# Optimization experiments

Measured on AMD Instinct MI355X. Metric: run time of the kernel, lower is better.

## Reference

```python
import jax, jax.numpy as jnp
import numpy as np

N_CLASSES = 18
NMS_PRE = 1000   # test_cfg.nms_pre, per level
K_NMS = 500      # per-class candidates entering greedy NMS
SCORE_THR = 0.01
IOU_THR = 0.5
LEVEL_NS = [600000, 300000, 150000, 75000]


def _decode(points, pred):
    # fcaf3d axis-aligned decode: pred = (dx-, dx+, dy-, dy+, dz-, dz+) >= 0
    cx = points[:, 0] + (pred[:, 1] - pred[:, 0]) / 2
    cy = points[:, 1] + (pred[:, 3] - pred[:, 2]) / 2
    cz = points[:, 2] + (pred[:, 5] - pred[:, 4]) / 2
    w = pred[:, 0] + pred[:, 1]
    l = pred[:, 2] + pred[:, 3]
    h = pred[:, 4] + pred[:, 5]
    return jnp.stack([cx, cy, cz, w, l, h], axis=-1)  # [N, 6]


def _iou3d(b):
    # axis-aligned 3D IoU, b: [K,6] (cx,cy,cz,w,l,h) -> [K,K]
    mn = b[:, :3] - b[:, 3:] / 2
    mx = b[:, :3] + b[:, 3:] / 2
    lt = jnp.maximum(mn[:, None, :], mn[None, :, :])
    rb = jnp.minimum(mx[:, None, :], mx[None, :, :])
    inter = jnp.clip(rb - lt, 0.0).prod(-1)
    vol = jnp.clip(mx - mn, 0.0).prod(-1)
    return inter / (vol[:, None] + vol[None, :] - inter + 1e-6)


def _level(centerness, bbox_pred, cls_score, points):
    # fused score: cls.sigmoid() * centerness.sigmoid()
    scores = jax.nn.sigmoid(cls_score) * jax.nn.sigmoid(centerness)  # [N,C]
    max_scores = scores.max(axis=1)
    _, ids = jax.lax.top_k(max_scores, NMS_PRE)  # per-level prefilter
    bboxes = _decode(points[ids], bbox_pred[ids])  # [NMS_PRE, 6]
    return bboxes, scores[ids]


def _nms_class(boxes, scores):
    # boxes [M,6], scores [M] for one class -> greedy NMS on top K_NMS
    valid = scores > SCORE_THR
    s = jnp.where(valid, scores, -1.0)
    sv, order = jax.lax.top_k(s, K_NMS)  # sorted desc
    b = boxes[order]
    v = sv > SCORE_THR
    iou = _iou3d(b)  # [K,K]
    idx = jnp.arange(K_NMS)

    def body(i, sup):
        alive = jnp.logical_not(sup[i])
        return sup | (alive & (iou[i] > IOU_THR) & (idx > i))

    sup = jax.lax.fori_loop(0, K_NMS, body, jnp.logical_not(v))
    keep = jnp.logical_not(sup) & v
    return b, sv, keep


def _forward(levels):
    mlvl_bboxes, mlvl_scores = [], []
    for (cn, bp, cs, pt) in levels:
        b, s = _level(cn, bp, cs, pt)
        mlvl_bboxes.append(b)
        mlvl_scores.append(s)
    bboxes = jnp.concatenate(mlvl_bboxes)  # [4*NMS_PRE, 6]
    scores = jnp.concatenate(mlvl_scores)  # [4*NMS_PRE, C]
    # per-class NMS (vmap over class dim)
    b, sv, keep = jax.vmap(_nms_class, in_axes=(None, 1))(bboxes, scores)
    labels = jnp.broadcast_to(jnp.arange(N_CLASSES, dtype=jnp.int32)[:, None], sv.shape)
    return (b.reshape(-1, 6), sv.reshape(-1), labels.reshape(-1), keep.reshape(-1))


def setup_inputs() -> dict:
    key = jax.random.key(0)
    out = {}
    for li, n in enumerate(LEVEL_NS):
        k1, k2, k3, k4, key = jax.random.split(key, 5)
        out[f'centerness{li}'] = jax.random.normal(k1, (n, 1), jnp.float32)
        out[f'bbox_pred{li}'] = jax.random.uniform(k2, (n, 6), jnp.float32)  # non-negative distances
        out[f'cls_score{li}'] = jax.random.normal(k3, (n, N_CLASSES), jnp.float32)
        out[f'points{li}'] = jax.random.normal(k4, (n, 3), jnp.float32) * 2.0
    return out


def reference(centerness0, bbox_pred0, cls_score0, points0,
              centerness1, bbox_pred1, cls_score1, points1,
              centerness2, bbox_pred2, cls_score2, points2,
              centerness3, bbox_pred3, cls_score3, points3):
    levels = [
        (centerness0, bbox_pred0, cls_score0, points0),
        (centerness1, bbox_pred1, cls_score1, points1),
        (centerness2, bbox_pred2, cls_score2, points2),
        (centerness3, bbox_pred3, cls_score3, points3),
    ]
    return _forward(levels)
```

## Files before the change

### kernel.cpp

```cpp
#include <hip/hip_runtime.h>
#include <math.h>

#define N_CLASSES 18
#define NMS_PRE   1000
#define K_NMS     500
#define POOL      4000
#define LIST_CAP  2048
#define NREP      16
#define NSUB      16
#define SUBCAP    (LIST_CAP/NSUB)
#define IOU_THR   0.5f
#define SCORE_THR 0.01f

typedef unsigned long long ull;

struct Ptrs {
  const float* cent[4];
  const float* bbox[4];
  const float* cls[4];
  const float* pts[4];
  int off[4];
  int ntot;
};

__device__ __forceinline__ unsigned int fsort(float f){
  unsigned int b = __float_as_uint(f);
  return (b & 0x80000000u) ? ~b : (b | 0x80000000u);
}
__device__ __forceinline__ float fsort_inv(unsigned int k){
  unsigned int b = (k & 0x80000000u) ? (k & 0x7FFFFFFFu) : ~k;
  return __uint_as_float(b);
}
__device__ __forceinline__ float sigmoidf_(float x){
  return 1.0f / (1.0f + expf(-x));
}
__device__ __forceinline__ int level_of(int f, const Ptrs& P){
  return (f >= P.off[3]) ? 3 : (f >= P.off[2]) ? 2 : (f >= P.off[1]) ? 1 : 0;
}

__device__ __forceinline__ ull cx_keep(ull mine, ull part, bool keep_hi){
  ull mx = mine > part ? mine : part;
  ull mn = mine > part ? part : mine;
  return keep_hi ? mx : mn;
}
__device__ __forceinline__ void cxpair(ull &a, ull &b, bool a_hi){
  ull mx = a > b ? a : b;
  ull mn = a > b ? b : a;
  a = a_hi ? mx : mn;
  b = a_hi ? mn : mx;
}

__global__ void __launch_bounds__(256) init_kernel(unsigned int* hist_rep, unsigned int* hist2,
                        unsigned int* scnt, ull* lists, unsigned int* state){
  int tid = blockIdx.x*256 + threadIdx.x;
  int stride = gridDim.x*256;
  for (int j = tid; j < NREP*4*2048; j += stride) hist_rep[j] = 0u;
  for (int j = tid; j < 4*2048; j += stride) hist2[j] = 0u;
  for (int j = tid; j < 4*NSUB*16; j += stride) scnt[j] = 0u;
  for (int j = tid; j < 4*LIST_CAP; j += stride) lists[j] = 0ull;
  if (tid < 4){
    state[2*tid]   = 0u;
    state[2*tid+1] = NMS_PRE;
  }
}

__global__ void __launch_bounds__(512) compute_keys(Ptrs P, unsigned int* keys,
                        unsigned int* hist_rep){
  __shared__ unsigned int lh[2048];
  int t = threadIdx.x;
  for (int j = t; j < 2048; j += 512) lh[j] = 0u;
  int ip = blockIdx.x*512 + t;
  int f  = ip << 1;
  int rep = blockIdx.x & (NREP - 1);
  bool valid = f < P.ntot;
  int f0 = blockIdx.x << 10;
  int fL = min(f0 + 1023, P.ntot - 1);
  bool uni = (level_of(f0, P) == level_of(fL, P)) && (f0 + 1023 < P.ntot);
  int Lb = level_of(f0, P);

  float mA = 0.f, mB = 0.f, cA = 0.f, cB = 0.f;
  int L = 0;
  if (valid){
    L = level_of(f, P);
    int i = f - P.off[L];
    const float4* q = (const float4*)(P.cls[L] + (size_t)i * N_CLASSES);
    float4 q0 = q[0], q1 = q[1], q2 = q[2], q3 = q[3], q4 = q[4];
    float4 q5 = q[5], q6 = q[6], q7 = q[7], q8 = q[8];
    mA = fmaxf(fmaxf(fmaxf(q0.x,q0.y), fmaxf(q0.z,q0.w)),
         fmaxf(fmaxf(fmaxf(q1.x,q1.y), fmaxf(q1.z,q1.w)),
         fmaxf(fmaxf(fmaxf(q2.x,q2.y), fmaxf(q2.z,q2.w)),
         fmaxf(fmaxf(fmaxf(q3.x,q3.y), fmaxf(q3.z,q3.w)),
               fmaxf(q4.x,q4.y)))));
    mB = fmaxf(fmaxf(q4.z,q4.w),
         fmaxf(fmaxf(fmaxf(q5.x,q5.y), fmaxf(q5.z,q5.w)),
         fmaxf(fmaxf(fmaxf(q6.x,q6.y), fmaxf(q6.z,q6.w)),
         fmaxf(fmaxf(fmaxf(q7.x,q7.y), fmaxf(q7.z,q7.w)),
               fmaxf(fmaxf(q8.x,q8.y), fmaxf(q8.z,q8.w))))));
    const float2 c2 = *(const float2*)(P.cent[L] + i);
    cA = c2.x; cB = c2.y;
  }
  __syncthreads();

  if (valid){
    float sA = sigmoidf_(mA) * sigmoidf_(cA);
    float sB = sigmoidf_(mB) * sigmoidf_(cB);
    unsigned int kA = fsort(sA), kB = fsort(sB);
    *(uint2*)(keys + f) = make_uint2(kA, kB);
    if (uni){
      atomicAdd(&lh[kA >> 21], 1u);
      atomicAdd(&lh[kB >> 21], 1u);
    } else {
      unsigned int* hb = hist_rep + ((rep*4) + L)*2048;
      atomicAdd(&hb[kA >> 21], 1u);
      atomicAdd(&hb[kB >> 21], 1u);
    }
  }
  __syncthreads();
  if (uni){
    unsigned int* hb = hist_rep + ((rep*4) + Lb)*2048;
    for (int j = t; j < 2048; j += 512){
      unsigned int v = lh[j];
      if (v) atomicAdd(&hb[j], v);
    }
  }
}

__global__ void __launch_bounds__(512) hist_level(Ptrs P, const unsigned int* keys,
                        const unsigned int* state, unsigned int* hist2){
  int ip = blockIdx.x*512 + threadIdx.x;
  int f = ip << 1;
  if (f < P.ntot){
    int L = level_of(f, P);
    uint2 kk = *(const uint2*)(keys + f);
    unsigned int Pfx = state[2*L];
    unsigned int hi = Pfx >> 21;
    if ((kk.x >> 21) == hi) atomicAdd(&hist2[L*2048 + ((kk.x >> 10) & 0x7FFu)], 1u);
    if ((kk.y >> 21) == hi) atomicAdd(&hist2[L*2048 + ((kk.y >> 10) & 0x7FFu)], 1u);
  }
}

__global__ void __launch_bounds__(256) scan_sel(const unsigned int* src, int nrep,
                        unsigned int* state, int pass){
  __shared__ unsigned int lhist[2048];
  int L = blockIdx.x, t = threadIdx.x;
  for (int j = t; j < 2048; j += 256){
    unsigned int s = 0u;
    if (nrep == NREP){
#pragma unroll
      for (int r = 0; r < NREP; ++r) s += src[((r*4) + L)*2048 + j];
    } else {
      s = src[L*2048 + j];
    }
    lhist[j] = s;
  }
  __syncthreads();
  if (t < 64){
    int lane = t;
    unsigned int krem = state[2*L + 1];
    unsigned int Pfx  = state[2*L];
    unsigned int carry = 0;
    for (int ch = 0; ch < 32; ++ch){
      unsigned int cnt = lhist[2047 - (ch*64 + lane)];
      unsigned int pfx = cnt;
#pragma unroll
      for (int off = 1; off < 64; off <<= 1){
        unsigned int u = __shfl_up(pfx, off);
        if (lane >= off) pfx += u;
      }
      unsigned int C = carry + pfx;
      ull bal = __ballot(C >= krem);
      if (bal){
        int fl2 = __ffsll(bal) - 1;
        unsigned int Cf = __shfl(C, fl2);
        unsigned int cf = __shfl(cnt, fl2);
        if (lane == 0){
          unsigned int b = (unsigned int)(2047 - (ch*64 + fl2));
          state[2*L]     = (pass == 0) ? (b << 21) : (Pfx | (b << 10));
          state[2*L + 1] = krem - (Cf - cf);
        }
        break;
      }
      carry = __shfl(C, 63);
    }
  }
}

__global__ void __launch_bounds__(512) compact_kernel(Ptrs P, const unsigned int* keys,
                        const unsigned int* state, unsigned int* scnt, ull* lists){
  int ip = blockIdx.x*512 + threadIdx.x;
  int f = ip << 1;
  if (f >= P.ntot) return;
  int L = level_of(f, P);
  uint2 kk = *(const uint2*)(keys + f);
  unsigned int T = state[2*L];
  unsigned int sub = (unsigned int)blockIdx.x & (NSUB - 1);
  if (kk.x >= T){
    unsigned int pos = atomicAdd(&scnt[(L*NSUB + sub)*16], 1u);
    if (pos < SUBCAP){
      unsigned int i = (unsigned int)(f - P.off[L]);
      lists[(size_t)L*LIST_CAP + sub*SUBCAP + pos] = ((ull)kk.x << 32) | (ull)(~i);
    }
  }
  if (kk.y >= T){
    unsigned int pos = atomicAdd(&scnt[(L*NSUB + sub)*16], 1u);
    if (pos < SUBCAP){
      unsigned int i = (unsigned int)(f + 1 - P.off[L]);
      lists[(size_t)L*LIST_CAP + sub*SUBCAP + pos] = ((ull)kk.y << 32) | (ull)(~i);
    }
  }
}

__global__ void __launch_bounds__(1024) sort_idx(const ull* lists, unsigned int* sidx){
  __shared__ ull buf[LIST_CAP];
  int L = blockIdx.x;
  int t = threadIdx.x;
  int e1 = t + 1024;
  const ull* src = lists + (size_t)L*LIST_CAP;
  ull v0 = src[t];
  ull v1 = src[e1];
  for (int k = 2; k <= 2048; k <<= 1){
    for (int j = k >> 1; j > 0; j >>= 1){
      bool hi0 = (((t  & j) == 0) == ((t  & k) == 0));
      bool hi1 = (((e1 & j) == 0) == ((e1 & k) == 0));
      if (j >= 1024){
        cxpair(v0, v1, hi0);
      } else if (j >= 64){
        __syncthreads();
        buf[t] = v0; buf[e1] = v1;
        __syncthreads();
        ull p0 = buf[t ^ j];
        ull p1 = buf[e1 ^ j];
        v0 = cx_keep(v0, p0, hi0);
        v1 = cx_keep(v1, p1, hi1);
      } else {
        ull p0 = __shfl_xor(v0, j);
        ull p1 = __shfl_xor(v1, j);
        v0 = cx_keep(v0, p0, hi0);
        v1 = cx_keep(v1, p1, hi1);
      }
    }
  }
  if (t < NMS_PRE) sidx[L*NMS_PRE + t] = ~((unsigned int)(v0 & 0xFFFFFFFFu));
}

__global__ void __launch_bounds__(64) gather_decode(Ptrs P, const unsigned int* sidx,
                        float* boxes_pool, float* scores_pool){
  int r = blockIdx.x*64 + threadIdx.x;
  if (r >= POOL) return;
  int L = r / NMS_PRE;
  unsigned int i = sidx[r];
  const float* bp = P.bbox[L] + (size_t)i * 6;
  const float* pp = P.pts[L]  + (size_t)i * 3;
  float p0 = bp[0], p1 = bp[1], p2 = bp[2], p3 = bp[3], p4 = bp[4], p5 = bp[5];
  float cx = pp[0] + (p1 - p0) * 0.5f;
  float cy = pp[1] + (p3 - p2) * 0.5f;
  float cz = pp[2] + (p5 - p4) * 0.5f;
  float w = p0 + p1, l = p2 + p3, h = p4 + p5;
  float* bo = boxes_pool + (size_t)r * 6;
  bo[0] = cx; bo[1] = cy; bo[2] = cz; bo[3] = w; bo[4] = l; bo[5] = h;
  float cs = sigmoidf_(P.cent[L][i]);
  const float* cl = P.cls[L] + (size_t)i * N_CLASSES;
#pragma unroll
  for (int c = 0; c < N_CLASSES; ++c)
    scores_pool[(size_t)c * POOL + r] = sigmoidf_(cl[c]) * cs;
}

__global__ void __launch_bounds__(1024) class_topk(const float* scores_pool, const float* boxes_pool,
                        float* out, float* aabb){
  __shared__ unsigned int keyS[4096];
  __shared__ ull comp[512];
  __shared__ unsigned int histS[256];
  __shared__ unsigned int wsum[16], wpre[16];
  __shared__ unsigned int sP, sK, sCnt;
  int c = blockIdx.x;
  int t = threadIdx.x;
  int w = t >> 6, lane = t & 63;

  for (int j = t; j < 4096; j += 1024){
    unsigned int k = 0u;
    if (j < POOL){
      float s = scores_pool[(size_t)c*POOL + j];
      float sval = (s > SCORE_THR) ? s : -1.0f;
      k = fsort(sval);
    }
    keyS[j] = k;
  }
  if (t == 0){ sP = 0u; sK = K_NMS; sCnt = 0u; }
  __syncthreads();

  for (int pass = 0; pass < 4; ++pass){
    int shift = 24 - 8*pass;
    if (t < 256) histS[t] = 0u;
    __syncthreads();
    unsigned int Pfx = sP;
    for (int j = t; j < 4096; j += 1024){
      unsigned int k = keyS[j];
      if ((((ull)(k ^ Pfx)) >> (shift + 8)) == 0ull)
        atomicAdd(&histS[(k >> shift) & 0xFFu], 1u);
    }
    __syncthreads();
    if (w == 0){
      unsigned int krem = sK;
      unsigned int carry = 0;
      for (int ch = 0; ch < 4; ++ch){
        unsigned int cnt = histS[255 - (ch*64 + lane)];
        unsigned int pfx = cnt;
#pragma unroll
        for (int off = 1; off < 64; off <<= 1){
          unsigned int u = __shfl_up(pfx, off);
          if (lane >= off) pfx += u;
        }
        unsigned int C = carry + pfx;
        ull bal = __ballot(C >= krem);
        if (bal){
          int fl = __ffsll(bal) - 1;
          unsigned int Cf = __shfl(C, fl);
          unsigned int cf = __shfl(cnt, fl);
          if (lane == 0){
            sP = Pfx | ((unsigned int)(255 - (ch*64 + fl)) << shift);
            sK = krem - (Cf - cf);
          }
          break;
        }
        carry = __shfl(C, 63);
      }
    }
    __syncthreads();
  }
  unsigned int T = sP, need = sK;

  unsigned int loc[4]; unsigned int ct = 0;
#pragma unroll
  for (int q = 0; q < 4; ++q){
    unsigned int k = keyS[4*t + q];
    loc[q] = k;
    ct += (k == T) ? 1u : 0u;
  }
  unsigned int inc = ct;
#pragma unroll
  for (int off = 1; off < 64; off <<= 1){
    unsigned int u = __shfl_up(inc, off);
    if (lane >= off) inc += u;
  }
  if (lane == 63) wsum[w] = inc;
  __syncthreads();
  if (t < 16){
    unsigned int v = wsum[t];
    unsigned int pincl = v;
#pragma unroll
    for (int off = 1; off < 16; off <<= 1){
      unsigned int u = __shfl_up(pincl, off);
      if (t >= off) pincl += u;
    }
    wpre[t] = pincl - v;
  }
  __syncthreads();
  unsigned int excl = wpre[w] + (inc - ct);

#pragma unroll
  for (int q = 0; q < 4; ++q){
    unsigned int k = loc[q];
    bool surv = false;
    if (k > T) surv = true;
    else if (k == T){ surv = (excl < need); excl += 1u; }
    if (surv){
      unsigned int pos = atomicAdd(&sCnt, 1u);
      if (pos < 512)
        comp[pos] = ((ull)k << 32) | (ull)(~(unsigned int)(4*t + q));
    }
  }
  __syncthreads();

  ull v0 = 0ull;
  if (t < 512 && t < (int)sCnt) v0 = comp[t];
  for (int k = 2; k <= 512; k <<= 1){
    for (int j = k >> 1; j > 0; j >>= 1){
      if (j >= 64){
        __syncthreads();
        if (t < 512) comp[t] = v0;
        __syncthreads();
        if (t < 512){
          ull p0 = comp[t ^ j];
          bool hi0 = (((t & j) == 0) == ((t & k) == 0));
          v0 = cx_keep(v0, p0, hi0);
        }
      } else {
        if (t < 512){
          ull p0 = __shfl_xor(v0, j);
          bool hi0 = (((t & j) == 0) == ((t & k) == 0));
          v0 = cx_keep(v0, p0, hi0);
        }
      }
    }
  }

  if (t < K_NMS){
    ull cm = v0;
    unsigned int j = ~((unsigned int)(cm & 0xFFFFFFFFu));
    float sval = fsort_inv((unsigned int)(cm >> 32));
    int o = c*K_NMS + t;
    const float* bp = boxes_pool + (size_t)j * 6;
    float b0 = bp[0], b1 = bp[1], b2 = bp[2], b3 = bp[3], b4 = bp[4], b5 = bp[5];
    float* ob = out + (size_t)o * 6;
    ob[0] = b0; ob[1] = b1; ob[2] = b2; ob[3] = b3; ob[4] = b4; ob[5] = b5;
    out[54000 + o] = sval;
    out[63000 + o] = (float)c;
    float mn0 = b0 - b3*0.5f, mx0 = b0 + b3*0.5f;
    float mn1 = b1 - b4*0.5f, mx1 = b1 + b4*0.5f;
    float mn2 = b2 - b5*0.5f, mx2 = b2 + b5*0.5f;
    float vol = fmaxf(mx0 - mn0, 0.f) * fmaxf(mx1 - mn1, 0.f) * fmaxf(mx2 - mn2, 0.f);
    float* ap = aabb + ((size_t)c*512 + t) * 8;
    ap[0] = mn0; ap[1] = mn1; ap[2] = mn2; ap[3] = mx0; ap[4] = mx1; ap[5] = mx2;
    ap[6] = vol; ap[7] = sval;
  }
}

__global__ void __launch_bounds__(512) nms_mask(const float* aabb, ull* maskG, ull* flagsG){
  __shared__ float smn0[512], smn1[512], smn2[512];
  __shared__ float smx0[512], smx1[512], smx2[512];
  __shared__ float svol[512];
  __shared__ ull rowbuf[64*8];
  int c = blockIdx.y, chunk = blockIdx.x;
  int t = threadIdx.x, w = t >> 6, lane = t & 63;
  float mn0 = 0.f, mn1 = 0.f, mn2 = 0.f, mx0 = 0.f, mx1 = 0.f, mx2 = 0.f, vol = 0.f;
  if (t < K_NMS){
    const float* ap = aabb + ((size_t)c*512 + t) * 8;
    mn0 = ap[0]; mn1 = ap[1]; mn2 = ap[2];
    mx0 = ap[3]; mx1 = ap[4]; mx2 = ap[5]; vol = ap[6];
  }
  smn0[t] = mn0; smn1[t] = mn1; smn2[t] = mn2;
  smx0[t] = mx0; smx1[t] = mx1; smx2[t] = mx2;
  svol[t] = vol;
  __syncthreads();
  int i0 = chunk * 64, i1 = min(i0 + 64, K_NMS);
  for (int i = i0; i < i1; ++i){
    float lt0 = fmaxf(smn0[i], mn0), lt1 = fmaxf(smn1[i], mn1), lt2 = fmaxf(smn2[i], mn2);
    float rb0 = fminf(smx0[i], mx0), rb1 = fminf(smx1[i], mx1), rb2 = fminf(smx2[i], mx2);
    float inter = fmaxf(rb0 - lt0, 0.f) * fmaxf(rb1 - lt1, 0.f) * fmaxf(rb2 - lt2, 0.f);
    float denom = svol[i] + vol - inter + 1e-6f;
    bool s = (t < K_NMS) && (t > i) && (inter / denom > IOU_THR);
    ull m = __ballot(s);
    if (lane == 0){
      maskG[((size_t)c*K_NMS + i)*8 + w] = m;
      rowbuf[(i - i0)*8 + w] = m;
    }
  }
  __syncthreads();
  if (t < 64){
    int r = i0 + t;
    bool nz = false;
    if (r < K_NMS){
      ull o = 0ull;
#pragma unroll
      for (int z = 0; z < 8; ++z) o |= rowbuf[t*8 + z];
      nz = (o != 0ull);
    }
    ull bal = __ballot(nz);
    if (t == 0) flagsG[(size_t)c*8 + chunk] = bal;
  }
}

__global__ void __launch_bounds__(512) nms_greedy(const float* aabb, const ull* maskG,
                        const ull* flagsG, float* keep_out){
  __shared__ ull maskS[K_NMS*8];
  __shared__ ull vbitsS[8], remS[8];
  int c = blockIdx.x, t = threadIdx.x, w = t >> 6, lane = t & 63;
  ull flg[8];
#pragma unroll
  for (int q = 0; q < 8; ++q) flg[q] = flagsG[(size_t)c*8 + q];
  for (int j = t; j < K_NMS*8; j += 512) maskS[j] = maskG[(size_t)c*K_NMS*8 + j];
  float sv = (t < K_NMS) ? aabb[((size_t)c*512 + t)*8 + 7] : -1.0f;
  ull vb = __ballot(sv > SCORE_THR);
  if (lane == 0) vbitsS[w] = vb;
  __syncthreads();
  if (w == 0){
    ull rem[8];
#pragma unroll
    for (int q = 0; q < 8; ++q) rem[q] = ~vbitsS[q];
#pragma unroll
    for (int q = 0; q < 8; ++q){
      ull cand = flg[q] & ~rem[q];
      while (cand){
        int b = __ffsll(cand) - 1;
        int i = q*64 + b;
#pragma unroll
        for (int z = 0; z < 8; ++z) rem[z] |= maskS[i*8 + z];
        ull above = (b < 63) ? (~0ull << (b + 1)) : 0ull;
        cand = flg[q] & ~rem[q] & above;
      }
    }
    if (lane == 0){
#pragma unroll
      for (int q = 0; q < 8; ++q) remS[q] = rem[q];
    }
  }
  __syncthreads();
  if (t < K_NMS)
    keep_out[c*K_NMS + t] = ((remS[t >> 6] >> (t & 63)) & 1ull) ? 0.0f : 1.0f;
}

extern "C" void kernel_launch(void* const* d_in, const int* in_sizes, int n_in,
                              void* d_out, int out_size, void* d_ws, size_t ws_size,
                              hipStream_t stream){
  Ptrs P;
  int off = 0;
  for (int L = 0; L < 4; ++L){
    P.cent[L] = (const float*)d_in[4*L + 0];
    P.bbox[L] = (const float*)d_in[4*L + 1];
    P.cls[L]  = (const float*)d_in[4*L + 2];
    P.pts[L]  = (const float*)d_in[4*L + 3];
    P.off[L]  = off;
    off += in_sizes[4*L + 0];
  }
  P.ntot = off;

  char* w = (char*)d_ws;
  size_t o = 0;
  auto alloc = [&](size_t bytes) -> char* {
    char* p = w + o;
    o = (o + bytes + 255) & ~(size_t)255;
    return p;
  };
  unsigned int* keys        = (unsigned int*)alloc((size_t)P.ntot * 4);
  unsigned int* hist_rep    = (unsigned int*)alloc((size_t)NREP * 4 * 2048 * 4);
  unsigned int* hist2       = (unsigned int*)alloc(4 * 2048 * 4);
  unsigned int* state       = (unsigned int*)alloc(4 * 2 * 4);
  unsigned int* scnt        = (unsigned int*)alloc(4 * NSUB * 16 * 4);
  ull* lists                = (ull*)alloc((size_t)4 * LIST_CAP * 8);
  unsigned int* sidx        = (unsigned int*)alloc((size_t)POOL * 4);
  float* boxes_pool         = (float*)alloc((size_t)POOL * 6 * 4);
  float* scores_pool        = (float*)alloc((size_t)N_CLASSES * POOL * 4);
  float* aabb               = (float*)alloc((size_t)N_CLASSES * 512 * 8 * 4);
  ull* maskG                = (ull*)alloc((size_t)N_CLASSES * K_NMS * 8 * 8);
  ull* flagsG               = (ull*)alloc((size_t)N_CLASSES * 8 * 8);

  float* out = (float*)d_out;
  int npairs = P.ntot >> 1;
  int pgrid = (npairs + 511) / 512;

  init_kernel<<<64, 256, 0, stream>>>(hist_rep, hist2, scnt, lists, state);
  compute_keys<<<pgrid, 512, 0, stream>>>(P, keys, hist_rep);
  scan_sel<<<4, 256, 0, stream>>>(hist_rep, NREP, state, 0);
  hist_level<<<pgrid, 512, 0, stream>>>(P, keys, state, hist2);
  scan_sel<<<4, 256, 0, stream>>>(hist2, 1, state, 1);
  compact_kernel<<<pgrid, 512, 0, stream>>>(P, keys, state, scnt, lists);
  sort_idx<<<4, 1024, 0, stream>>>(lists, sidx);
  gather_decode<<<(POOL + 63)/64, 64, 0, stream>>>(P, sidx, boxes_pool, scores_pool);
  class_topk<<<N_CLASSES, 1024, 0, stream>>>(scores_pool, boxes_pool, out, aabb);
  nms_mask<<<dim3(8, N_CLASSES), 512, 0, stream>>>(aabb, maskG, flagsG);
  nms_greedy<<<N_CLASSES, 512, 0, stream>>>(aabb, maskG, flagsG, out + 72000);
}
```

Before: 264.6 us.

## Fold radix-select scans into histogram/compact kernels and fuse gather-decode into class top-k

Drops the two small scan_sel launches. Each block of the histogram and compaction kernels now recomputes the per-level threshold scan itself from the replicated histograms, which removes the global state buffer. The gather_decode kernel and its score and box pool buffers are removed: class_topk recomputes sigmoid scores per class and decodes boxes directly from the inputs through sidx. This cuts three kernel launches and their serial dependencies, at the cost of every block re-reading the 16 replicated histograms and redundant sigmoid work across the 18 class blocks.

```diff
diff --git a/kernel.cpp b/kernel.cpp
--- a/kernel.cpp
+++ b/kernel.cpp
@@ -51,17 +51,13 @@
 }
 
 __global__ void __launch_bounds__(256) init_kernel(unsigned int* hist_rep, unsigned int* hist2,
-                        unsigned int* scnt, ull* lists, unsigned int* state){
+                        unsigned int* scnt, ull* lists){
   int tid = blockIdx.x*256 + threadIdx.x;
   int stride = gridDim.x*256;
   for (int j = tid; j < NREP*4*2048; j += stride) hist_rep[j] = 0u;
   for (int j = tid; j < 4*2048; j += stride) hist2[j] = 0u;
   for (int j = tid; j < 4*NSUB*16; j += stride) scnt[j] = 0u;
   for (int j = tid; j < 4*LIST_CAP; j += stride) lists[j] = 0ull;
-  if (tid < 4){
-    state[2*tid]   = 0u;
-    state[2*tid+1] = NMS_PRE;
-  }
 }
 
 __global__ void __launch_bounds__(512) compute_keys(Ptrs P, unsigned int* keys,
@@ -125,74 +121,140 @@
   }
 }
 
-__global__ void __launch_bounds__(512) hist_level(Ptrs P, const unsigned int* keys,
-                        const unsigned int* state, unsigned int* hist2){
-  int ip = blockIdx.x*512 + threadIdx.x;
+__global__ void __launch_bounds__(512) hist_scan0(Ptrs P, const unsigned int* keys,
+                        const unsigned int* hist_rep, unsigned int* hist2){
+  __shared__ unsigned int lhist[2048];
+  __shared__ unsigned int binS[4];
+  int t = threadIdx.x, lane = t & 63, w = t >> 6;
+  if (t < 4) binS[t] = 0xFFFFFFFFu;
+  int ip = blockIdx.x*512 + t;
   int f = ip << 1;
+  int f0 = blockIdx.x << 10;
+  int fL = min(f0 + 1023, P.ntot - 1);
+  int L0 = level_of(f0, P), L1 = level_of(fL, P);
+  for (int pass = 0; pass < 2; ++pass){
+    if (pass && L1 == L0) break;
+    int L = pass ? L1 : L0;
+    __syncthreads();
+    for (int j = t; j < 2048; j += 512){
+      unsigned int s = 0u;
+#pragma unroll
+      for (int r = 0; r < NREP; ++r) s += hist_rep[((r*4) + L)*2048 + j];
+      lhist[j] = s;
+    }
+    __syncthreads();
+    if (w == 0){
+      unsigned int krem = NMS_PRE, carry = 0;
+      for (int ch = 0; ch < 32; ++ch){
+        unsigned int cnt = lhist[2047 - (ch*64 + lane)];
+        unsigned int pfx = cnt;
+#pragma unroll
+        for (int off = 1; off < 64; off <<= 1){
+          unsigned int u = __shfl_up(pfx, off);
+          if (lane >= off) pfx += u;
+        }
+        unsigned int C = carry + pfx;
+        ull bal = __ballot(C >= krem);
+        if (bal){
+          int fl2 = __ffsll(bal) - 1;
+          if (lane == 0) binS[L] = (unsigned int)(2047 - (ch*64 + fl2));
+          break;
+        }
+        carry = __shfl(C, 63);
+      }
+    }
+  }
+  __syncthreads();
   if (f < P.ntot){
     int L = level_of(f, P);
+    unsigned int B = binS[L];
     uint2 kk = *(const uint2*)(keys + f);
-    unsigned int Pfx = state[2*L];
-    unsigned int hi = Pfx >> 21;
-    if ((kk.x >> 21) == hi) atomicAdd(&hist2[L*2048 + ((kk.x >> 10) & 0x7FFu)], 1u);
-    if ((kk.y >> 21) == hi) atomicAdd(&hist2[L*2048 + ((kk.y >> 10) & 0x7FFu)], 1u);
-  }
-}
-
-__global__ void __launch_bounds__(256) scan_sel(const unsigned int* src, int nrep,
-                        unsigned int* state, int pass){
+    if ((kk.x >> 21) == B) atomicAdd(&hist2[L*2048 + ((kk.x >> 10) & 0x7FFu)], 1u);
+    if ((kk.y >> 21) == B) atomicAdd(&hist2[L*2048 + ((kk.y >> 10) & 0x7FFu)], 1u);
+  }
+}
+
+__global__ void __launch_bounds__(512) compact_scan(Ptrs P, const unsigned int* keys,
+                        const unsigned int* hist_rep, const unsigned int* hist2,
+                        unsigned int* scnt, ull* lists){
   __shared__ unsigned int lhist[2048];
-  int L = blockIdx.x, t = threadIdx.x;
-  for (int j = t; j < 2048; j += 256){
-    unsigned int s = 0u;
-    if (nrep == NREP){
-#pragma unroll
-      for (int r = 0; r < NREP; ++r) s += src[((r*4) + L)*2048 + j];
-    } else {
-      s = src[L*2048 + j];
-    }
-    lhist[j] = s;
-  }
-  __syncthreads();
-  if (t < 64){
-    int lane = t;
-    unsigned int krem = state[2*L + 1];
-    unsigned int Pfx  = state[2*L];
-    unsigned int carry = 0;
-    for (int ch = 0; ch < 32; ++ch){
-      unsigned int cnt = lhist[2047 - (ch*64 + lane)];
-      unsigned int pfx = cnt;
-#pragma unroll
-      for (int off = 1; off < 64; off <<= 1){
-        unsigned int u = __shfl_up(pfx, off);
-        if (lane >= off) pfx += u;
-      }
-      unsigned int C = carry + pfx;
-      ull bal = __ballot(C >= krem);
-      if (bal){
-        int fl2 = __ffsll(bal) - 1;
-        unsigned int Cf = __shfl(C, fl2);
-        unsigned int cf = __shfl(cnt, fl2);
-        if (lane == 0){
-          unsigned int b = (unsigned int)(2047 - (ch*64 + fl2));
-          state[2*L]     = (pass == 0) ? (b << 21) : (Pfx | (b << 10));
-          state[2*L + 1] = krem - (Cf - cf);
-        }
-        break;
-      }
-      carry = __shfl(C, 63);
-    }
-  }
-}
-
-__global__ void __launch_bounds__(512) compact_kernel(Ptrs P, const unsigned int* keys,
-                        const unsigned int* state, unsigned int* scnt, ull* lists){
-  int ip = blockIdx.x*512 + threadIdx.x;
+  __shared__ unsigned int TS[4];
+  __shared__ unsigned int b0S, krem0S;
+  int t = threadIdx.x, lane = t & 63, w = t >> 6;
+  if (t < 4) TS[t] = 0xFFFFFFFFu;
+  int ip = blockIdx.x*512 + t;
   int f = ip << 1;
+  int f0 = blockIdx.x << 10;
+  int fL = min(f0 + 1023, P.ntot - 1);
+  int L0 = level_of(f0, P), L1 = level_of(fL, P);
+  for (int pass = 0; pass < 2; ++pass){
+    if (pass && L1 == L0) break;
+    int L = pass ? L1 : L0;
+    __syncthreads();
+    for (int j = t; j < 2048; j += 512){
+      unsigned int s = 0u;
+#pragma unroll
+      for (int r = 0; r < NREP; ++r) s += hist_rep[((r*4) + L)*2048 + j];
+      lhist[j] = s;
+    }
+    __syncthreads();
+    if (w == 0){
+      unsigned int krem = NMS_PRE, carry = 0;
+      for (int ch = 0; ch < 32; ++ch){
+        unsigned int cnt = lhist[2047 - (ch*64 + lane)];
+        unsigned int pfx = cnt;
+#pragma unroll
+        for (int off = 1; off < 64; off <<= 1){
+          unsigned int u = __shfl_up(pfx, off);
+          if (lane >= off) pfx += u;
+        }
+        unsigned int C = carry + pfx;
+        ull bal = __ballot(C >= krem);
+        if (bal){
+          int fl2 = __ffsll(bal) - 1;
+          unsigned int Cf = __shfl(C, fl2);
+          unsigned int cf = __shfl(cnt, fl2);
+          if (lane == 0){
+            b0S = (unsigned int)(2047 - (ch*64 + fl2));
+            krem0S = krem - (Cf - cf);
+          }
+          break;
+        }
+        carry = __shfl(C, 63);
+      }
+    }
+    __syncthreads();
+    unsigned int Pfx = b0S << 21;
+    unsigned int krem1 = krem0S;
+    for (int j = t; j < 2048; j += 512) lhist[j] = hist2[L*2048 + j];
+    __syncthreads();
+    if (w == 0){
+      unsigned int krem = krem1, carry = 0;
+      for (int ch = 0; ch < 32; ++ch){
+        unsigned int cnt = lhist[2047 - (ch*64 + lane)];
+        unsigned int pfx = cnt;
+#pragma unroll
+        for (int off = 1; off < 64; off <<= 1){
+          unsigned int u = __shfl_up(pfx, off);
+          if (lane >= off) pfx += u;
+        }
+        unsigned int C = carry + pfx;
+        ull bal = __ballot(C >= krem);
+        if (bal){
+          int fl2 = __ffsll(bal) - 1;
+          if (lane == 0)
+            TS[L] = Pfx | ((unsigned int)(2047 - (ch*64 + fl2)) << 10);
+          break;
+        }
+        carry = __shfl(C, 63);
+      }
+    }
+  }
+  __syncthreads();
   if (f >= P.ntot) return;
   int L = level_of(f, P);
+  unsigned int T = TS[L];
   uint2 kk = *(const uint2*)(keys + f);
-  unsigned int T = state[2*L];
   unsigned int sub = (unsigned int)blockIdx.x & (NSUB - 1);
   if (kk.x >= T){
     unsigned int pos = atomicAdd(&scnt[(L*NSUB + sub)*16], 1u);
@@ -243,29 +305,7 @@
   if (t < NMS_PRE) sidx[L*NMS_PRE + t] = ~((unsigned int)(v0 & 0xFFFFFFFFu));
 }
 
-__global__ void __launch_bounds__(64) gather_decode(Ptrs P, const unsigned int* sidx,
-                        float* boxes_pool, float* scores_pool){
-  int r = blockIdx.x*64 + threadIdx.x;
-  if (r >= POOL) return;
-  int L = r / NMS_PRE;
-  unsigned int i = sidx[r];
-  const float* bp = P.bbox[L] + (size_t)i * 6;
-  const float* pp = P.pts[L]  + (size_t)i * 3;
-  float p0 = bp[0], p1 = bp[1], p2 = bp[2], p3 = bp[3], p4 = bp[4], p5 = bp[5];
-  float cx = pp[0] + (p1 - p0) * 0.5f;
-  float cy = pp[1] + (p3 - p2) * 0.5f;
-  float cz = pp[2] + (p5 - p4) * 0.5f;
-  float w = p0 + p1, l = p2 + p3, h = p4 + p5;
-  float* bo = boxes_pool + (size_t)r * 6;
-  bo[0] = cx; bo[1] = cy; bo[2] = cz; bo[3] = w; bo[4] = l; bo[5] = h;
-  float cs = sigmoidf_(P.cent[L][i]);
-  const float* cl = P.cls[L] + (size_t)i * N_CLASSES;
-#pragma unroll
-  for (int c = 0; c < N_CLASSES; ++c)
-    scores_pool[(size_t)c * POOL + r] = sigmoidf_(cl[c]) * cs;
-}
-
-__global__ void __launch_bounds__(1024) class_topk(const float* scores_pool, const float* boxes_pool,
+__global__ void __launch_bounds__(1024) class_topk(Ptrs P, const unsigned int* sidx,
                         float* out, float* aabb){
   __shared__ unsigned int keyS[4096];
   __shared__ ull comp[512];
@@ -279,7 +319,9 @@
   for (int j = t; j < 4096; j += 1024){
     unsigned int k = 0u;
     if (j < POOL){
-      float s = scores_pool[(size_t)c*POOL + j];
+      int L = j / NMS_PRE;
+      unsigned int i = sidx[j];
+      float s = sigmoidf_(P.cls[L][(size_t)i * N_CLASSES + c]) * sigmoidf_(P.cent[L][i]);
       float sval = (s > SCORE_THR) ? s : -1.0f;
       k = fsort(sval);
     }
@@ -396,11 +438,18 @@
 
   if (t < K_NMS){
     ull cm = v0;
-    unsigned int j = ~((unsigned int)(cm & 0xFFFFFFFFu));
+    unsigned int jj = ~((unsigned int)(cm & 0xFFFFFFFFu));
     float sval = fsort_inv((unsigned int)(cm >> 32));
     int o = c*K_NMS + t;
-    const float* bp = boxes_pool + (size_t)j * 6;
-    float b0 = bp[0], b1 = bp[1], b2 = bp[2], b3 = bp[3], b4 = bp[4], b5 = bp[5];
+    int L = (int)jj / NMS_PRE;
+    unsigned int i = sidx[jj];
+    const float* bp = P.bbox[L] + (size_t)i * 6;
+    const float* pp = P.pts[L]  + (size_t)i * 3;
+    float p0 = bp[0], p1 = bp[1], p2 = bp[2], p3 = bp[3], p4 = bp[4], p5 = bp[5];
+    float b0 = pp[0] + (p1 - p0) * 0.5f;
+    float b1 = pp[1] + (p3 - p2) * 0.5f;
+    float b2 = pp[2] + (p5 - p4) * 0.5f;
+    float b3 = p0 + p1, b4 = p2 + p3, b5 = p4 + p5;
     float* ob = out + (size_t)o * 6;
     ob[0] = b0; ob[1] = b1; ob[2] = b2; ob[3] = b3; ob[4] = b4; ob[5] = b5;
     out[54000 + o] = sval;
@@ -524,12 +573,9 @@
   unsigned int* keys        = (unsigned int*)alloc((size_t)P.ntot * 4);
   unsigned int* hist_rep    = (unsigned int*)alloc((size_t)NREP * 4 * 2048 * 4);
   unsigned int* hist2       = (unsigned int*)alloc(4 * 2048 * 4);
-  unsigned int* state       = (unsigned int*)alloc(4 * 2 * 4);
   unsigned int* scnt        = (unsigned int*)alloc(4 * NSUB * 16 * 4);
   ull* lists                = (ull*)alloc((size_t)4 * LIST_CAP * 8);
   unsigned int* sidx        = (unsigned int*)alloc((size_t)POOL * 4);
-  float* boxes_pool         = (float*)alloc((size_t)POOL * 6 * 4);
-  float* scores_pool        = (float*)alloc((size_t)N_CLASSES * POOL * 4);
   float* aabb               = (float*)alloc((size_t)N_CLASSES * 512 * 8 * 4);
   ull* maskG                = (ull*)alloc((size_t)N_CLASSES * K_NMS * 8 * 8);
   ull* flagsG               = (ull*)alloc((size_t)N_CLASSES * 8 * 8);
@@ -538,15 +584,12 @@
   int npairs = P.ntot >> 1;
   int pgrid = (npairs + 511) / 512;
 
-  init_kernel<<<64, 256, 0, stream>>>(hist_rep, hist2, scnt, lists, state);
+  init_kernel<<<64, 256, 0, stream>>>(hist_rep, hist2, scnt, lists);
   compute_keys<<<pgrid, 512, 0, stream>>>(P, keys, hist_rep);
-  scan_sel<<<4, 256, 0, stream>>>(hist_rep, NREP, state, 0);
-  hist_level<<<pgrid, 512, 0, stream>>>(P, keys, state, hist2);
-  scan_sel<<<4, 256, 0, stream>>>(hist2, 1, state, 1);
-  compact_kernel<<<pgrid, 512, 0, stream>>>(P, keys, state, scnt, lists);
+  hist_scan0<<<pgrid, 512, 0, stream>>>(P, keys, hist_rep, hist2);
+  compact_scan<<<pgrid, 512, 0, stream>>>(P, keys, hist_rep, hist2, scnt, lists);
   sort_idx<<<4, 1024, 0, stream>>>(lists, sidx);
-  gather_decode<<<(POOL + 63)/64, 64, 0, stream>>>(P, sidx, boxes_pool, scores_pool);
-  class_topk<<<N_CLASSES, 1024, 0, stream>>>(scores_pool, boxes_pool, out, aabb);
+  class_topk<<<N_CLASSES, 1024, 0, stream>>>(P, sidx, out, aabb);
   nms_mask<<<dim3(8, N_CLASSES), 512, 0, stream>>>(aabb, maskG, flagsG);
   nms_greedy<<<N_CLASSES, 512, 0, stream>>>(aabb, maskG, flagsG, out + 72000);
 }
```

Result: slower. 299.1 us (+13.0%).
